# Performance work log

Hardware: AMD Instinct MI355X
Metric: run time of the kernel (lower is better)

The kernel has to match this reference:

```python
import jax, jax.numpy as jnp
import numpy as np

N, E, D, L = 50000, 800000, 128, 3

def setup_inputs() -> dict:
    key = jax.random.key(0)
    ks = jax.random.split(key, 6)
    X = jax.random.normal(ks[0], (N, D), dtype=jnp.float32)
    edge_index = jax.random.randint(ks[1], (2, E), 0, N, dtype=jnp.int64)
    eps = jax.random.normal(ks[2], (L,), dtype=jnp.float32)
    # Glorot-ish scaling for stability
    W1 = jax.random.normal(ks[3], (L, D, D), dtype=jnp.float32) / np.sqrt(D)
    b1 = jnp.zeros((L, D), dtype=jnp.float32)
    W2 = jax.random.normal(ks[4], (L, D, D), dtype=jnp.float32) / np.sqrt(D)
    b2 = jnp.zeros((L, D), dtype=jnp.float32)
    return {"X": X, "edge_index": edge_index, "eps": eps,
            "W1": W1, "b1": b1, "W2": W2, "b2": b2}

def reference(X, edge_index, eps, W1, b1, W2, b2):
    src = edge_index[0]  # message sources j (flow source_to_target)
    dst = edge_index[1]  # aggregation targets i
    n = X.shape[0]
    for i in range(L):  # fixed small layer loop
        X0 = X
        # propagate: gather X_j over edges, scatter-add to targets
        S = jax.ops.segment_sum(X[src], dst, num_segments=n)  # [N, D]
        Z = (1.0 + eps[i]) * X + S
        # MLP: Linear -> ReLU -> Linear
        H = jnp.maximum(Z @ W1[i] + b1[i], 0.0)
        X = H @ W2[i] + b2[i]
        X = X + X0  # residual=True
    return X
```

## Files before the change

### kernel.cpp

```cpp
#include <hip/hip_runtime.h>

#define NN 50000
#define NE 800000
#define DD 128
#define NL 3
#define ELLW 64
#define MT_TOTAL (NN / 16)
#define MT_PER_XCD 391
#define NODES_PER_XCD (MT_PER_XCD * 16)
#define SCAT_BLKS (MT_PER_XCD * 8)
#define SCAT_CHUNK 2048
#define PACK_BLKS ((6 * 2048 + 255) / 256)
#define INIT_BLKS 3128

typedef short bf16x8 __attribute__((ext_vector_type(8)));
typedef float f32x4 __attribute__((ext_vector_type(4)));
typedef _Float16 half8 __attribute__((ext_vector_type(8)));
typedef unsigned short u16x8 __attribute__((ext_vector_type(8)));

__device__ __forceinline__ unsigned short f2bf(float x) {
  unsigned u = __float_as_uint(x);
  u += 0x7FFFu + ((u >> 16) & 1u);
  return (unsigned short)(u >> 16);
}
__device__ __forceinline__ float bf2f(unsigned short h) {
  return __uint_as_float(((unsigned)h) << 16);
}
__device__ __forceinline__ void cvt8(const float* zz, bf16x8* hi, bf16x8* lo) {
#pragma unroll
  for (int i = 0; i < 8; ++i) {
    unsigned short h = f2bf(zz[i]);
    (*hi)[i] = (short)h;
    (*lo)[i] = (short)f2bf(zz[i] - bf2f(h));
  }
}

__global__ __launch_bounds__(256) void prologue_k(
    const int* __restrict__ ei, int* __restrict__ cnt, unsigned short* __restrict__ ell,
    const float* __restrict__ W1, const float* __restrict__ W2,
    unsigned short* __restrict__ Wp,
    const float* __restrict__ X, _Float16* __restrict__ Xh)
{
  int b = blockIdx.x;
  if (b < SCAT_BLKS) {
    int g = b & 7, chunk = b >> 3;
    int lo = g * NODES_PER_XCD, hi = lo + NODES_PER_XCD;
    int base = chunk * SCAT_CHUNK + threadIdx.x * 8;
    if (base + 7 < NE) {
      int4 d0 = *(const int4*)(ei + NE + base);
      int4 d1 = *(const int4*)(ei + NE + base + 4);
      int4 s0 = *(const int4*)(ei + base);
      int4 s1 = *(const int4*)(ei + base + 4);
      int dd[8] = {d0.x, d0.y, d0.z, d0.w, d1.x, d1.y, d1.z, d1.w};
      int ss[8] = {s0.x, s0.y, s0.z, s0.w, s1.x, s1.y, s1.z, s1.w};
#pragma unroll
      for (int i = 0; i < 8; ++i) {
        int d = dd[i];
        if (d >= lo && d < hi) {
          int pos = atomicAdd(&cnt[d], 1);
          if (pos < ELLW) ell[(size_t)d * ELLW + pos] = (unsigned short)ss[i];
        }
      }
    } else {
      for (int e = base; e < NE; ++e) {
        int d = ei[NE + e];
        if (d >= lo && d < hi) {
          int pos = atomicAdd(&cnt[d], 1);
          if (pos < ELLW) ell[(size_t)d * ELLW + pos] = (unsigned short)ei[e];
        }
      }
    }
  } else if (b < SCAT_BLKS + PACK_BLKS) {
    int t = (b - SCAT_BLKS) * 256 + threadIdx.x;
    if (t < 6 * 2048) {
      int m = t >> 11;
      int rem = t & 2047;
      int l = rem & 63;
      int ntks = rem >> 6;
      int ks = ntks & 3, nt = ntks >> 2;
      const float* W = (m < 3) ? (W1 + (size_t)m * DD * DD) : (W2 + (size_t)(m - 3) * DD * DD);
      int col = nt * 16 + (l & 15);
      int k0 = ks * 32 + (l >> 4) * 8;
      unsigned short* hi = Wp + (size_t)m * 2 * DD * DD + (size_t)rem * 8;
      unsigned short* lo = hi + DD * DD;
#pragma unroll
      for (int i = 0; i < 8; ++i) {
        float w = W[(size_t)(k0 + i) * DD + col];
        unsigned short h = f2bf(w);
        hi[i] = h;
        lo[i] = f2bf(w - bf2f(h));
      }
    }
  } else {
    int bb = b - SCAT_BLKS - PACK_BLKS;
    int g = bb & 7, ii = bb >> 3;
    int mt = g * MT_PER_XCD + ii;
    if (mt < MT_TOTAL) {
      size_t base = (size_t)mt * 16 * DD + threadIdx.x * 8;
      const float4* p = (const float4*)(X + base);
      float4 a = p[0], bb2 = p[1];
      half8 h;
      h[0] = (_Float16)a.x;   h[1] = (_Float16)a.y;   h[2] = (_Float16)a.z;   h[3] = (_Float16)a.w;
      h[4] = (_Float16)bb2.x; h[5] = (_Float16)bb2.y; h[6] = (_Float16)bb2.z; h[7] = (_Float16)bb2.w;
      *(half8*)(Xh + base) = h;
    }
  }
}

template<int OUT_F32>
__global__ __launch_bounds__(256) void fused_layer_k(
    const _Float16* __restrict__ Xh_in,
    const int* __restrict__ cnt, const unsigned short* __restrict__ ell,
    const float* __restrict__ eps, int layer,
    const unsigned short* __restrict__ Wp1, const float* __restrict__ b1,
    const unsigned short* __restrict__ Wp2, const float* __restrict__ b2,
    float* __restrict__ Xf_out, _Float16* __restrict__ Xh_out)
{
  __shared__ float ztile[16 * 132];
  __shared__ unsigned short rtile[16 * 136];
  const int mt = (blockIdx.x & 7) * MT_PER_XCD + (blockIdx.x >> 3);
  if (mt >= MT_TOTAL) return;
  const int w = threadIdx.x >> 6, l = threadIdx.x & 63;
  const int c = l & 15, grp = l >> 4;

  {
    const float e1 = 1.0f + eps[layer];
    const int nl = w * 4 + grp;
    const int node = mt * 16 + nl;
    int deg = cnt[node]; deg = deg > ELLW ? ELLW : deg;
    const unsigned short* el = ell + (size_t)node * ELLW;
    const u16x8* el8 = (const u16x8*)el;
    half8 sv = *(const half8*)(Xh_in + (size_t)node * DD + c * 8);
    *(u16x8*)(rtile + nl * 136 + c * 8) = *(const u16x8*)&sv;
    half8 acch = (half8)(_Float16)0.0f;
    int nf8 = deg >> 3;
    u16x8 nxt;
    if (nf8) nxt = el8[0];
    for (int t = 0; t < nf8; ++t) {
      u16x8 cur = nxt;
      if (t + 1 < nf8) nxt = el8[t + 1];
      half8 v0 = *(const half8*)(Xh_in + (size_t)cur[0] * DD + c * 8);
      half8 v1 = *(const half8*)(Xh_in + (size_t)cur[1] * DD + c * 8);
      half8 v2 = *(const half8*)(Xh_in + (size_t)cur[2] * DD + c * 8);
      half8 v3 = *(const half8*)(Xh_in + (size_t)cur[3] * DD + c * 8);
      half8 v4 = *(const half8*)(Xh_in + (size_t)cur[4] * DD + c * 8);
      half8 v5 = *(const half8*)(Xh_in + (size_t)cur[5] * DD + c * 8);
      half8 v6 = *(const half8*)(Xh_in + (size_t)cur[6] * DD + c * 8);
      half8 v7 = *(const half8*)(Xh_in + (size_t)cur[7] * DD + c * 8);
      half8 s = ((v0 + v1) + (v2 + v3)) + ((v4 + v5) + (v6 + v7));
      acch += s;
    }
    for (int j = nf8 * 8; j < deg; ++j) {
      half8 v = *(const half8*)(Xh_in + (size_t)el[j] * DD + c * 8);
      acch += v;
    }
    float acc[8];
#pragma unroll
    for (int i = 0; i < 8; ++i) acc[i] = fmaf(e1, (float)sv[i], (float)acch[i]);
    float* dst = ztile + nl * 132 + c * 8;
    *(float4*)dst = make_float4(acc[0], acc[1], acc[2], acc[3]);
    *(float4*)(dst + 4) = make_float4(acc[4], acc[5], acc[6], acc[7]);
  }
  __syncthreads();

  f32x4 acc1[2];
#pragma unroll
  for (int nt = 0; nt < 2; ++nt) acc1[nt] = (f32x4){0.f, 0.f, 0.f, 0.f};
  {
    const float* arow = ztile + (l & 15) * 132;
    const unsigned short* Whi = Wp1;
    const unsigned short* Wlo = Wp1 + DD * DD;
#pragma unroll
    for (int ks = 0; ks < 4; ++ks) {
      const float* zp = arow + ks * 32 + grp * 8;
      float zz[8] = {zp[0], zp[1], zp[2], zp[3], zp[4], zp[5], zp[6], zp[7]};
      bf16x8 ahi, alo; cvt8(zz, &ahi, &alo);
#pragma unroll
      for (int nt = 0; nt < 2; ++nt) {
        int ntb = w * 2 + nt;
        size_t off = ((size_t)(ntb * 4 + ks) * 64 + l) * 8;
        bf16x8 bhi = *(const bf16x8*)(Whi + off);
        bf16x8 blo = *(const bf16x8*)(Wlo + off);
        acc1[nt] = __builtin_amdgcn_mfma_f32_16x16x32_bf16(ahi, bhi, acc1[nt], 0, 0, 0);
        acc1[nt] = __builtin_amdgcn_mfma_f32_16x16x32_bf16(ahi, blo, acc1[nt], 0, 0, 0);
        acc1[nt] = __builtin_amdgcn_mfma_f32_16x16x32_bf16(alo, bhi, acc1[nt], 0, 0, 0);
      }
    }
  }
  __syncthreads();

  {
#pragma unroll
    for (int nt = 0; nt < 2; ++nt) {
      int ntb = w * 2 + nt;
      float bv = b1[ntb * 16 + c];
#pragma unroll
      for (int r = 0; r < 4; ++r)
        ztile[(grp * 4 + r) * 132 + ntb * 16 + c] = fmaxf(acc1[nt][r] + bv, 0.f);
    }
  }
  __syncthreads();

  f32x4 acc2[2];
#pragma unroll
  for (int nt = 0; nt < 2; ++nt) acc2[nt] = (f32x4){0.f, 0.f, 0.f, 0.f};
  {
    const float* arow = ztile + (l & 15) * 132;
    const unsigned short* Whi = Wp2;
    const unsigned short* Wlo = Wp2 + DD * DD;
#pragma unroll
    for (int ks = 0; ks < 4; ++ks) {
      const float* hp = arow + ks * 32 + grp * 8;
      float hh[8] = {hp[0], hp[1], hp[2], hp[3], hp[4], hp[5], hp[6], hp[7]};
      bf16x8 ahi, alo; cvt8(hh, &ahi, &alo);
#pragma unroll
      for (int nt = 0; nt < 2; ++nt) {
        int ntb = w * 2 + nt;
        size_t off = ((size_t)(ntb * 4 + ks) * 64 + l) * 8;
        bf16x8 bhi = *(const bf16x8*)(Whi + off);
        bf16x8 blo = *(const bf16x8*)(Wlo + off);
        acc2[nt] = __builtin_amdgcn_mfma_f32_16x16x32_bf16(ahi, bhi, acc2[nt], 0, 0, 0);
        acc2[nt] = __builtin_amdgcn_mfma_f32_16x16x32_bf16(ahi, blo, acc2[nt], 0, 0, 0);
        acc2[nt] = __builtin_amdgcn_mfma_f32_16x16x32_bf16(alo, bhi, acc2[nt], 0, 0, 0);
      }
    }
#pragma unroll
    for (int nt = 0; nt < 2; ++nt) {
      int ntb = w * 2 + nt;
      int col = ntb * 16 + c;
      float bv = b2[col];
#pragma unroll
      for (int r = 0; r < 4; ++r) {
        int row = grp * 4 + r;
        int node = mt * 16 + row;
        size_t idx = (size_t)node * DD + col;
        unsigned short rb = rtile[row * 136 + col];
        float rv = (float)(*(_Float16*)&rb);
        float v = acc2[nt][r] + bv + rv;
        if (OUT_F32) Xf_out[idx] = v;
        else         Xh_out[idx] = (_Float16)v;
      }
    }
  }
}

extern "C" void kernel_launch(void* const* d_in, const int* in_sizes, int n_in,
                              void* d_out, int out_size, void* d_ws, size_t ws_size,
                              hipStream_t stream) {
  const float* X   = (const float*)d_in[0];
  const int*   ei  = (const int*)d_in[1];
  const float* eps = (const float*)d_in[2];
  const float* W1  = (const float*)d_in[3];
  const float* b1  = (const float*)d_in[4];
  const float* W2  = (const float*)d_in[5];
  const float* b2  = (const float*)d_in[6];
  float* Xout = (float*)d_out;

  char* ws = (char*)d_ws;
  size_t off = 0;
  int* cnt = (int*)(ws + off); off += 256 * (((size_t)NN * 4 + 255) / 256);
  unsigned short* ell = (unsigned short*)(ws + off); off += (size_t)NN * ELLW * 2;
  unsigned short* Wp = (unsigned short*)(ws + off); off += (size_t)6 * 2 * DD * DD * 2;
  off = 256 * ((off + 255) / 256);
  _Float16* Xh0 = (_Float16*)(ws + off); off += (size_t)NN * DD * 2;
  _Float16* Xh1 = (_Float16*)(ws + off); off += (size_t)NN * DD * 2;

  hipMemsetAsync(cnt, 0, NN * 4, stream);
  prologue_k<<<SCAT_BLKS + PACK_BLKS + INIT_BLKS, 256, 0, stream>>>(
      ei, cnt, ell, W1, W2, Wp, X, Xh0);

  const int fgrid = MT_PER_XCD * 8;
  fused_layer_k<0><<<fgrid, 256, 0, stream>>>(Xh0, cnt, ell, eps, 0,
      Wp + (size_t)0 * 2 * DD * DD, b1 + 0 * DD,
      Wp + (size_t)3 * 2 * DD * DD, b2 + 0 * DD, nullptr, Xh1);
  fused_layer_k<0><<<fgrid, 256, 0, stream>>>(Xh1, cnt, ell, eps, 1,
      Wp + (size_t)1 * 2 * DD * DD, b1 + 1 * DD,
      Wp + (size_t)4 * 2 * DD * DD, b2 + 1 * DD, nullptr, Xh0);
  fused_layer_k<1><<<fgrid, 256, 0, stream>>>(Xh0, cnt, ell, eps, 2,
      Wp + (size_t)2 * 2 * DD * DD, b1 + 2 * DD,
      Wp + (size_t)5 * 2 * DD * DD, b2 + 2 * DD, Xout, nullptr);
}
```

Before: 187.3 us.

## Split fused layer into separate aggregation and MLP kernels with fp16 Z buffer

Un-fuses each layer's gather-aggregate from its two-layer MLP. A standalone aggregation kernel writes Z in fp16 to a new workspace buffer, and an MLP kernel reads Z straight from global memory plus the residual. The aim is to keep the irregular, latency-bound gather from sharing blocks with the MFMA work and LDS, so each kernel can run at its own occupancy. The cost is three extra launches per run and an extra write plus read of an N×D fp16 buffer per layer. Z is also rounded to fp16 where it was previously kept in fp32, which loses precision.

```diff
diff --git a/kernel.cpp b/kernel.cpp
--- a/kernel.cpp
+++ b/kernel.cpp
@@ -107,73 +107,87 @@
   }
 }
 
-template<int OUT_F32>
-__global__ __launch_bounds__(256) void fused_layer_k(
+__global__ __launch_bounds__(256) void agg_k(
     const _Float16* __restrict__ Xh_in,
     const int* __restrict__ cnt, const unsigned short* __restrict__ ell,
     const float* __restrict__ eps, int layer,
+    _Float16* __restrict__ Z)
+{
+  const int mt = (blockIdx.x & 7) * MT_PER_XCD + (blockIdx.x >> 3);
+  if (mt >= MT_TOTAL) return;
+  const int l = threadIdx.x & 63, w = threadIdx.x >> 6;
+  const int c = l & 15, grp = l >> 4;
+  const float e1 = 1.0f + eps[layer];
+  const int nl = w * 4 + grp;
+  const int node = mt * 16 + nl;
+  int deg = cnt[node]; deg = deg > ELLW ? ELLW : deg;
+  const unsigned short* el = ell + (size_t)node * ELLW;
+  const u16x8* el8 = (const u16x8*)el;
+  half8 sv = *(const half8*)(Xh_in + (size_t)node * DD + c * 8);
+  half8 acch = (half8)(_Float16)0.0f;
+  int nf8 = deg >> 3;
+  u16x8 nxt;
+  if (nf8) nxt = el8[0];
+  for (int t = 0; t < nf8; ++t) {
+    u16x8 cur = nxt;
+    if (t + 1 < nf8) nxt = el8[t + 1];
+    half8 v0 = *(const half8*)(Xh_in + (size_t)cur[0] * DD + c * 8);
+    half8 v1 = *(const half8*)(Xh_in + (size_t)cur[1] * DD + c * 8);
+    half8 v2 = *(const half8*)(Xh_in + (size_t)cur[2] * DD + c * 8);
+    half8 v3 = *(const half8*)(Xh_in + (size_t)cur[3] * DD + c * 8);
+    half8 v4 = *(const half8*)(Xh_in + (size_t)cur[4] * DD + c * 8);
+    half8 v5 = *(const half8*)(Xh_in + (size_t)cur[5] * DD + c * 8);
+    half8 v6 = *(const half8*)(Xh_in + (size_t)cur[6] * DD + c * 8);
+    half8 v7 = *(const half8*)(Xh_in + (size_t)cur[7] * DD + c * 8);
+    half8 s = ((v0 + v1) + (v2 + v3)) + ((v4 + v5) + (v6 + v7));
+    acch += s;
+  }
+  for (int j = nf8 * 8; j < deg; ++j) {
+    half8 v = *(const half8*)(Xh_in + (size_t)el[j] * DD + c * 8);
+    acch += v;
+  }
+  half8 z;
+#pragma unroll
+  for (int i = 0; i < 8; ++i)
+    z[i] = (_Float16)fmaf(e1, (float)sv[i], (float)acch[i]);
+  *(half8*)(Z + (size_t)node * DD + c * 8) = z;
+}
+
+template<int OUT_F32>
+__global__ __launch_bounds__(256) void mlp_k(
+    const _Float16* __restrict__ Z, const _Float16* __restrict__ Xh_resid,
     const unsigned short* __restrict__ Wp1, const float* __restrict__ b1,
     const unsigned short* __restrict__ Wp2, const float* __restrict__ b2,
     float* __restrict__ Xf_out, _Float16* __restrict__ Xh_out)
 {
   __shared__ float ztile[16 * 132];
-  __shared__ unsigned short rtile[16 * 136];
+  __shared__ unsigned short rh[16 * 136];
   const int mt = (blockIdx.x & 7) * MT_PER_XCD + (blockIdx.x >> 3);
   if (mt >= MT_TOTAL) return;
-  const int w = threadIdx.x >> 6, l = threadIdx.x & 63;
+  const int t = threadIdx.x;
+  const int w = t >> 6, l = t & 63;
   const int c = l & 15, grp = l >> 4;
 
   {
-    const float e1 = 1.0f + eps[layer];
-    const int nl = w * 4 + grp;
-    const int node = mt * 16 + nl;
-    int deg = cnt[node]; deg = deg > ELLW ? ELLW : deg;
-    const unsigned short* el = ell + (size_t)node * ELLW;
-    const u16x8* el8 = (const u16x8*)el;
-    half8 sv = *(const half8*)(Xh_in + (size_t)node * DD + c * 8);
-    *(u16x8*)(rtile + nl * 136 + c * 8) = *(const u16x8*)&sv;
-    half8 acch = (half8)(_Float16)0.0f;
-    int nf8 = deg >> 3;
-    u16x8 nxt;
-    if (nf8) nxt = el8[0];
-    for (int t = 0; t < nf8; ++t) {
-      u16x8 cur = nxt;
-      if (t + 1 < nf8) nxt = el8[t + 1];
-      half8 v0 = *(const half8*)(Xh_in + (size_t)cur[0] * DD + c * 8);
-      half8 v1 = *(const half8*)(Xh_in + (size_t)cur[1] * DD + c * 8);
-      half8 v2 = *(const half8*)(Xh_in + (size_t)cur[2] * DD + c * 8);
-      half8 v3 = *(const half8*)(Xh_in + (size_t)cur[3] * DD + c * 8);
-      half8 v4 = *(const half8*)(Xh_in + (size_t)cur[4] * DD + c * 8);
-      half8 v5 = *(const half8*)(Xh_in + (size_t)cur[5] * DD + c * 8);
-      half8 v6 = *(const half8*)(Xh_in + (size_t)cur[6] * DD + c * 8);
-      half8 v7 = *(const half8*)(Xh_in + (size_t)cur[7] * DD + c * 8);
-      half8 s = ((v0 + v1) + (v2 + v3)) + ((v4 + v5) + (v6 + v7));
-      acch += s;
-    }
-    for (int j = nf8 * 8; j < deg; ++j) {
-      half8 v = *(const half8*)(Xh_in + (size_t)el[j] * DD + c * 8);
-      acch += v;
-    }
-    float acc[8];
-#pragma unroll
-    for (int i = 0; i < 8; ++i) acc[i] = fmaf(e1, (float)sv[i], (float)acch[i]);
-    float* dst = ztile + nl * 132 + c * 8;
-    *(float4*)dst = make_float4(acc[0], acc[1], acc[2], acc[3]);
-    *(float4*)(dst + 4) = make_float4(acc[4], acc[5], acc[6], acc[7]);
-  }
-  __syncthreads();
+    int row = t >> 4, cb = t & 15;
+    u16x8 v = *(const u16x8*)((const unsigned short*)Xh_resid +
+                              (size_t)(mt * 16 + row) * DD + cb * 8);
+    *(u16x8*)(rh + row * 136 + cb * 8) = v;
+  }
 
   f32x4 acc1[2];
 #pragma unroll
   for (int nt = 0; nt < 2; ++nt) acc1[nt] = (f32x4){0.f, 0.f, 0.f, 0.f};
   {
-    const float* arow = ztile + (l & 15) * 132;
+    const _Float16* zrow = Z + (size_t)(mt * 16 + (l & 15)) * DD;
     const unsigned short* Whi = Wp1;
     const unsigned short* Wlo = Wp1 + DD * DD;
 #pragma unroll
     for (int ks = 0; ks < 4; ++ks) {
-      const float* zp = arow + ks * 32 + grp * 8;
-      float zz[8] = {zp[0], zp[1], zp[2], zp[3], zp[4], zp[5], zp[6], zp[7]};
+      half8 zh8 = *(const half8*)(zrow + ks * 32 + grp * 8);
+      float zz[8];
+#pragma unroll
+      for (int i = 0; i < 8; ++i) zz[i] = (float)zh8[i];
       bf16x8 ahi, alo; cvt8(zz, &ahi, &alo);
 #pragma unroll
       for (int nt = 0; nt < 2; ++nt) {
@@ -187,8 +201,6 @@
       }
     }
   }
-  __syncthreads();
-
   {
 #pragma unroll
     for (int nt = 0; nt < 2; ++nt) {
@@ -234,7 +246,7 @@
         int row = grp * 4 + r;
         int node = mt * 16 + row;
         size_t idx = (size_t)node * DD + col;
-        unsigned short rb = rtile[row * 136 + col];
+        unsigned short rb = rh[row * 136 + col];
         float rv = (float)(*(_Float16*)&rb);
         float v = acc2[nt][r] + bv + rv;
         if (OUT_F32) Xf_out[idx] = v;
@@ -264,19 +276,23 @@
   off = 256 * ((off + 255) / 256);
   _Float16* Xh0 = (_Float16*)(ws + off); off += (size_t)NN * DD * 2;
   _Float16* Xh1 = (_Float16*)(ws + off); off += (size_t)NN * DD * 2;
+  _Float16* Zb  = (_Float16*)(ws + off); off += (size_t)NN * DD * 2;
 
   hipMemsetAsync(cnt, 0, NN * 4, stream);
   prologue_k<<<SCAT_BLKS + PACK_BLKS + INIT_BLKS, 256, 0, stream>>>(
       ei, cnt, ell, W1, W2, Wp, X, Xh0);
 
   const int fgrid = MT_PER_XCD * 8;
-  fused_layer_k<0><<<fgrid, 256, 0, stream>>>(Xh0, cnt, ell, eps, 0,
+  agg_k<<<fgrid, 256, 0, stream>>>(Xh0, cnt, ell, eps, 0, Zb);
+  mlp_k<0><<<fgrid, 256, 0, stream>>>(Zb, Xh0,
       Wp + (size_t)0 * 2 * DD * DD, b1 + 0 * DD,
       Wp + (size_t)3 * 2 * DD * DD, b2 + 0 * DD, nullptr, Xh1);
-  fused_layer_k<0><<<fgrid, 256, 0, stream>>>(Xh1, cnt, ell, eps, 1,
+  agg_k<<<fgrid, 256, 0, stream>>>(Xh1, cnt, ell, eps, 1, Zb);
+  mlp_k<0><<<fgrid, 256, 0, stream>>>(Zb, Xh1,
       Wp + (size_t)1 * 2 * DD * DD, b1 + 1 * DD,
       Wp + (size_t)4 * 2 * DD * DD, b2 + 1 * DD, nullptr, Xh0);
-  fused_layer_k<1><<<fgrid, 256, 0, stream>>>(Xh0, cnt, ell, eps, 2,
+  agg_k<<<fgrid, 256, 0, stream>>>(Xh0, cnt, ell, eps, 2, Zb);
+  mlp_k<1><<<fgrid, 256, 0, stream>>>(Zb, Xh0,
       Wp + (size_t)2 * 2 * DD * DD, b1 + 2 * DD,
       Wp + (size_t)5 * 2 * DD * DD, b2 + 2 * DD, Xout, nullptr);
 }
```

After: 216.8 us. 15.8% more time.

## Sort nodes by degree within each XCD partition to balance gather loops

Applied to the files above, without the earlier changes.

Adds histogram, prefix and placement kernels that build a permutation of nodes grouped by in-degree inside each XCD partition, with the degree packed into the upper bits of each entry. The fused layer kernel reads node id and degree from this permutation, so nodes handled together have similar neighbour counts. This is meant to cut divergence and idle lanes in the gather loop, which runs to the largest degree among a wave's nodes. The cost is three extra small kernel launches plus a memset, and output rows are now written in permuted rather than sequential order.

```diff
diff --git a/kernel.cpp b/kernel.cpp
--- a/kernel.cpp
+++ b/kernel.cpp
@@ -12,6 +12,7 @@
 #define SCAT_CHUNK 2048
 #define PACK_BLKS ((6 * 2048 + 255) / 256)
 #define INIT_BLKS 3128
+#define NODE_BLKS ((NN + 255) / 256)
 
 typedef short bf16x8 __attribute__((ext_vector_type(8)));
 typedef float f32x4 __attribute__((ext_vector_type(4)));
@@ -107,10 +108,46 @@
   }
 }
 
+__global__ __launch_bounds__(256) void hist_k(const int* __restrict__ cnt,
+                                              int* __restrict__ hist) {
+  __shared__ int lh[8 * 65];
+  for (int i = threadIdx.x; i < 8 * 65; i += 256) lh[i] = 0;
+  __syncthreads();
+  int n = blockIdx.x * 256 + threadIdx.x;
+  if (n < NN) {
+    int deg = cnt[n]; deg = deg > ELLW ? ELLW : deg;
+    int part = n / NODES_PER_XCD;
+    atomicAdd(&lh[part * 65 + deg], 1);
+  }
+  __syncthreads();
+  for (int i = threadIdx.x; i < 8 * 65; i += 256)
+    if (lh[i]) atomicAdd(&hist[i], lh[i]);
+}
+
+__global__ __launch_bounds__(64) void prefix_k(const int* __restrict__ hist,
+                                               int* __restrict__ cursor) {
+  int g = threadIdx.x;
+  if (g < 8) {
+    int base = g * NODES_PER_XCD;
+    for (int b = 0; b <= ELLW; ++b) { cursor[g * 65 + b] = base; base += hist[g * 65 + b]; }
+  }
+}
+
+__global__ __launch_bounds__(256) void place_k(const int* __restrict__ cnt,
+                                               int* __restrict__ cursor,
+                                               int* __restrict__ perm) {
+  int n = blockIdx.x * 256 + threadIdx.x;
+  if (n >= NN) return;
+  int deg = cnt[n]; deg = deg > ELLW ? ELLW : deg;
+  int part = n / NODES_PER_XCD;
+  int rank = atomicAdd(&cursor[part * 65 + deg], 1);
+  perm[rank] = n | (deg << 16);
+}
+
 template<int OUT_F32>
 __global__ __launch_bounds__(256) void fused_layer_k(
     const _Float16* __restrict__ Xh_in,
-    const int* __restrict__ cnt, const unsigned short* __restrict__ ell,
+    const int* __restrict__ perm, const unsigned short* __restrict__ ell,
     const float* __restrict__ eps, int layer,
     const unsigned short* __restrict__ Wp1, const float* __restrict__ b1,
     const unsigned short* __restrict__ Wp2, const float* __restrict__ b2,
@@ -126,8 +163,9 @@
   {
     const float e1 = 1.0f + eps[layer];
     const int nl = w * 4 + grp;
-    const int node = mt * 16 + nl;
-    int deg = cnt[node]; deg = deg > ELLW ? ELLW : deg;
+    const int pe = perm[mt * 16 + nl];
+    const int node = pe & 0xFFFF;
+    const int deg = pe >> 16;
     const unsigned short* el = ell + (size_t)node * ELLW;
     const u16x8* el8 = (const u16x8*)el;
     half8 sv = *(const half8*)(Xh_in + (size_t)node * DD + c * 8);
@@ -232,8 +270,8 @@
 #pragma unroll
       for (int r = 0; r < 4; ++r) {
         int row = grp * 4 + r;
-        int node = mt * 16 + row;
-        size_t idx = (size_t)node * DD + col;
+        int onode = perm[mt * 16 + row] & 0xFFFF;
+        size_t idx = (size_t)onode * DD + col;
         unsigned short rb = rtile[row * 136 + col];
         float rv = (float)(*(_Float16*)&rb);
         float v = acc2[nt][r] + bv + rv;
@@ -258,25 +296,32 @@
 
   char* ws = (char*)d_ws;
   size_t off = 0;
-  int* cnt = (int*)(ws + off); off += 256 * (((size_t)NN * 4 + 255) / 256);
+  int* cnt    = (int*)(ws + off); off += 256 * (((size_t)NN * 4 + 255) / 256);
+  int* hist   = (int*)(ws + off); off += 256 * ((8 * 65 * 4 + 255) / 256);
+  int* cursor = (int*)(ws + off); off += 256 * ((8 * 65 * 4 + 255) / 256);
+  int* perm   = (int*)(ws + off); off += 256 * (((size_t)(MT_PER_XCD * 8 * 16) * 4 + 255) / 256);
   unsigned short* ell = (unsigned short*)(ws + off); off += (size_t)NN * ELLW * 2;
-  unsigned short* Wp = (unsigned short*)(ws + off); off += (size_t)6 * 2 * DD * DD * 2;
+  unsigned short* Wp  = (unsigned short*)(ws + off); off += (size_t)6 * 2 * DD * DD * 2;
   off = 256 * ((off + 255) / 256);
   _Float16* Xh0 = (_Float16*)(ws + off); off += (size_t)NN * DD * 2;
   _Float16* Xh1 = (_Float16*)(ws + off); off += (size_t)NN * DD * 2;
 
   hipMemsetAsync(cnt, 0, NN * 4, stream);
+  hipMemsetAsync(hist, 0, 8 * 65 * 4, stream);
   prologue_k<<<SCAT_BLKS + PACK_BLKS + INIT_BLKS, 256, 0, stream>>>(
       ei, cnt, ell, W1, W2, Wp, X, Xh0);
+  hist_k<<<NODE_BLKS, 256, 0, stream>>>(cnt, hist);
+  prefix_k<<<1, 64, 0, stream>>>(hist, cursor);
+  place_k<<<NODE_BLKS, 256, 0, stream>>>(cnt, cursor, perm);
 
   const int fgrid = MT_PER_XCD * 8;
-  fused_layer_k<0><<<fgrid, 256, 0, stream>>>(Xh0, cnt, ell, eps, 0,
+  fused_layer_k<0><<<fgrid, 256, 0, stream>>>(Xh0, perm, ell, eps, 0,
       Wp + (size_t)0 * 2 * DD * DD, b1 + 0 * DD,
       Wp + (size_t)3 * 2 * DD * DD, b2 + 0 * DD, nullptr, Xh1);
-  fused_layer_k<0><<<fgrid, 256, 0, stream>>>(Xh1, cnt, ell, eps, 1,
+  fused_layer_k<0><<<fgrid, 256, 0, stream>>>(Xh1, perm, ell, eps, 1,
       Wp + (size_t)1 * 2 * DD * DD, b1 + 1 * DD,
       Wp + (size_t)4 * 2 * DD * DD, b2 + 1 * DD, nullptr, Xh0);
-  fused_layer_k<1><<<fgrid, 256, 0, stream>>>(Xh0, cnt, ell, eps, 2,
+  fused_layer_k<1><<<fgrid, 256, 0, stream>>>(Xh0, perm, ell, eps, 2,
       Wp + (size_t)2 * 2 * DD * DD, b1 + 2 * DD,
       Wp + (size_t)5 * 2 * DD * DD, b2 + 2 * DD, Xout, nullptr);
 }
```

Measured after the change: 198.2 us. 5.8% more time.
